# Kernel optimization log

Measured on AMD Instinct MI355X. Metric: run time of the kernel, lower is better.

The kernel has to match this reference:

```python
import jax, jax.numpy as jnp
import numpy as np

EPSILON = 1e-8
N, M, D = 8192, 8192, 128
NUM_LABELS = 10


def setup_inputs() -> dict:
    key = jax.random.key(0)
    k1, k2, k3 = jax.random.split(key, 3)
    a = jax.random.normal(k1, (N, D), dtype=jnp.float32)
    b = jax.random.normal(k2, (M, D), dtype=jnp.float32)
    labels_for_a = jax.random.randint(k3, (N,), 0, NUM_LABELS, dtype=jnp.int64)
    return {"a": a, "b": b, "labels_for_a": labels_for_a}


def reference(a, b, labels_for_a):
    d = a.shape[1]
    # p: [n, m] scaled similarity
    p = jnp.matmul(a, b.T) / jnp.sqrt(jnp.float32(d))
    ab = jax.nn.softmax(p, axis=1)        # [n, m] walk a->b
    ba = jax.nn.softmax(p.T, axis=1)      # [m, n] walk b->a
    aba = jnp.matmul(ab, ba)              # [n, n] round-trip probability
    # label-equality targets, normalized per row
    labels = labels_for_a[None, :]
    is_same_label = (labels == labels.T).astype(jnp.float32)  # [n, n]
    label_count = is_same_label.sum(axis=1, keepdims=True)
    targets = is_same_label / label_count
    walker_loss = -(targets * jnp.log(EPSILON + aba)).sum(axis=1).mean(axis=0)
    # visit loss: uniform target over b
    visit_probability = ab.mean(axis=0)   # [m]
    m = b.shape[0]
    uniform = jnp.float32(1.0 / m)
    visit_loss = -(uniform * jnp.log(EPSILON + visit_probability)).sum(axis=0)
    return (walker_loss, visit_loss)
```

## Files before the change

### kernel.cpp

```cpp
#include <hip/hip_runtime.h>


typedef __attribute__((ext_vector_type(8))) short bf16x8;
typedef __attribute__((ext_vector_type(4))) float f32x4;

#define NROW 8192
#define DIM 128
#define NLAB 10
#define EPSf 1e-8f
#define SF 0.35709582f
#define SPLIT 4
#define NPAIR 36
#define SPSTRIDE (360 * 16384)

#define O_WA 0
#define O_VA 8
#define O_CNT 64
#define O_OFF 128
#define O_SIDX 256
#define O_PS 33280
#define O_CS 557568
#define O_VK 590336
#define O_CV 623104
#define O_CKS 655872
#define O_ABF 688640
#define O_BBF 2785792
#define O_E 4882944
#define O_SP 139100672

__device__ __forceinline__ unsigned short f2bf(float f) {
  unsigned u = __builtin_bit_cast(unsigned, f);
  u += 0x7fffu + ((u >> 16) & 1u);
  return (unsigned short)(u >> 16);
}
__device__ __forceinline__ float bf2f(unsigned short s) {
  unsigned u = ((unsigned)s) << 16;
  return __builtin_bit_cast(float, u);
}

__global__ __launch_bounds__(256) void k_bucket(const int* __restrict__ lab,
                                                int* cnt, int* offs, int* sidx,
                                                double* wa, double* va,
                                                float* cs, float* vk) {
  __shared__ int lc[NLAB], lcur[NLAB];
  int tid = threadIdx.x;
  if (tid < NLAB) lc[tid] = 0;
  __syncthreads();
  for (int i = tid; i < NROW; i += 256) {
    int l = lab[i]; l = l < 0 ? 0 : (l > 9 ? 9 : l);
    atomicAdd(&lc[l], 1);
  }
  for (int i = tid; i < NROW; i += 256) { cs[i] = 0.f; vk[i] = 0.f; }
  __syncthreads();
  if (tid == 0) {
    int run = 0;
    for (int l = 0; l < NLAB; ++l) { cnt[l] = lc[l]; offs[l] = run; lcur[l] = run; run += lc[l]; }
    *wa = 0.0; *va = 0.0;
  }
  __syncthreads();
  for (int i = tid; i < NROW; i += 256) {
    int l = lab[i]; l = l < 0 ? 0 : (l > 9 ? 9 : l);
    int p = atomicAdd(&lcur[l], 1);
    sidx[p] = i;
  }
}

__global__ __launch_bounds__(256) void k_convert(const float* __restrict__ X,
                                                 unsigned short* __restrict__ Y) {
  int i = (blockIdx.x * 256 + threadIdx.x) * 8;
  f32x4 a = *(const f32x4*)(X + i);
  f32x4 b = *(const f32x4*)(X + i + 4);
  bf16x8 o;
  o[0] = (short)f2bf(a[0] * SF); o[1] = (short)f2bf(a[1] * SF);
  o[2] = (short)f2bf(a[2] * SF); o[3] = (short)f2bf(a[3] * SF);
  o[4] = (short)f2bf(b[0] * SF); o[5] = (short)f2bf(b[1] * SF);
  o[6] = (short)f2bf(b[2] * SF); o[7] = (short)f2bf(b[3] * SF);
  *(bf16x8*)(Y + i) = o;
}

__global__ __launch_bounds__(256, 2) void k_stats(const unsigned short* __restrict__ Abf,
                                                  const unsigned short* __restrict__ Bbf,
                                                  const int* __restrict__ sidx,
                                                  float* __restrict__ ps,
                                                  float* __restrict__ CS) {
  __shared__ int gidx[128];
  int tid = threadIdx.x;
  if (tid < 128) gidx[tid] = sidx[blockIdx.x * 128 + tid];
  __syncthreads();
  int wave = tid >> 6, lane = tid & 63;
  int wrow = wave >> 1, wcol = wave & 1;
  int m = lane & 15, quad = lane >> 4;
  bf16x8 af[4][4];
#pragma unroll
  for (int mi = 0; mi < 4; ++mi) {
    int gi = gidx[wrow * 64 + mi * 16 + m];
#pragma unroll
    for (int ks = 0; ks < 4; ++ks)
      af[mi][ks] = *(const bf16x8*)(Abf + gi * DIM + ks * 32 + quad * 8);
  }
  float tsum[4][4];
#pragma unroll
  for (int mi = 0; mi < 4; ++mi)
#pragma unroll
    for (int r = 0; r < 4; ++r) tsum[mi][r] = 0.f;
  int p0 = blockIdx.x * 128 + wrow * 64;
  for (int t = 0; t < 8; ++t) {
    int c0 = blockIdx.y * 1024 + t * 128 + wcol * 64;
    bf16x8 bfr[4][4];
#pragma unroll
    for (int ni = 0; ni < 4; ++ni)
#pragma unroll
      for (int ks = 0; ks < 4; ++ks)
        bfr[ni][ks] = *(const bf16x8*)(Bbf + (c0 + ni * 16 + m) * DIM + ks * 32 + quad * 8);
    f32x4 acc[4][4];
#pragma unroll
    for (int mi = 0; mi < 4; ++mi)
#pragma unroll
      for (int ni = 0; ni < 4; ++ni) acc[mi][ni] = (f32x4){0.f, 0.f, 0.f, 0.f};
#pragma unroll
    for (int ks = 0; ks < 4; ++ks)
#pragma unroll
      for (int mi = 0; mi < 4; ++mi)
#pragma unroll
        for (int ni = 0; ni < 4; ++ni)
          acc[mi][ni] = __builtin_amdgcn_mfma_f32_16x16x32_bf16(af[mi][ks], bfr[ni][ks], acc[mi][ni], 0, 0, 0);
    float csum[4] = {0.f, 0.f, 0.f, 0.f};
#pragma unroll
    for (int mi = 0; mi < 4; ++mi)
#pragma unroll
      for (int ni = 0; ni < 4; ++ni)
#pragma unroll
        for (int r = 0; r < 4; ++r) {
          float e = __builtin_amdgcn_exp2f(acc[mi][ni][r]);
          tsum[mi][r] += e;
          csum[ni] += e;
        }
#pragma unroll
    for (int ni = 0; ni < 4; ++ni) {
      csum[ni] += __shfl_xor(csum[ni], 16);
      csum[ni] += __shfl_xor(csum[ni], 32);
    }
    if (lane < 16) {
#pragma unroll
      for (int ni = 0; ni < 4; ++ni) atomicAdd(&CS[c0 + ni * 16 + lane], csum[ni]);
    }
  }
#pragma unroll
  for (int off = 1; off < 16; off <<= 1)
#pragma unroll
    for (int mi = 0; mi < 4; ++mi)
#pragma unroll
      for (int r = 0; r < 4; ++r) tsum[mi][r] += __shfl_xor(tsum[mi][r], off);
  if (m == 0) {
#pragma unroll
    for (int mi = 0; mi < 4; ++mi)
#pragma unroll
      for (int r = 0; r < 4; ++r)
        ps[(blockIdx.y * 2 + wcol) * NROW + p0 + mi * 16 + quad * 4 + r] = tsum[mi][r];
  }
}

__global__ __launch_bounds__(256) void k_mstats(const float* __restrict__ ps,
                                                const float* __restrict__ CS,
                                                float* __restrict__ CVs,
                                                float* __restrict__ CKS) {
  int i = blockIdx.x * 256 + threadIdx.x;
  float s = 0.f;
#pragma unroll
  for (int t = 0; t < 16; ++t) s += ps[t * NROW + i];
  CVs[i] = 1.f / s;
  CKS[i] = rsqrtf(CS[i]);
}

__global__ __launch_bounds__(256, 2) void k_fill(const unsigned short* __restrict__ Abf,
                                                 const unsigned short* __restrict__ Bbf,
                                                 const int* __restrict__ sidx,
                                                 const float* __restrict__ CVs,
                                                 const float* __restrict__ CKS,
                                                 unsigned short* __restrict__ E,
                                                 float* __restrict__ VK) {
  __shared__ int gidx[128];
  int tid = threadIdx.x;
  if (tid < 128) gidx[tid] = sidx[blockIdx.x * 128 + tid];
  __syncthreads();
  int wave = tid >> 6, lane = tid & 63;
  int wrow = wave >> 1, wcol = wave & 1;
  int m = lane & 15, quad = lane >> 4;
  int p0 = blockIdx.x * 128 + wrow * 64;
  bf16x8 af[4][4];
  float cv16[4][4];
#pragma unroll
  for (int mi = 0; mi < 4; ++mi) {
    int gi = gidx[wrow * 64 + mi * 16 + m];
#pragma unroll
    for (int ks = 0; ks < 4; ++ks)
      af[mi][ks] = *(const bf16x8*)(Abf + gi * DIM + ks * 32 + quad * 8);
#pragma unroll
    for (int r = 0; r < 4; ++r) cv16[mi][r] = CVs[p0 + mi * 16 + quad * 4 + r];
  }
  for (int t = 0; t < 8; ++t) {
    int c0 = blockIdx.y * 1024 + t * 128 + wcol * 64;
    bf16x8 bfr[4][4];
    float ck4[4];
#pragma unroll
    for (int ni = 0; ni < 4; ++ni) {
      ck4[ni] = CKS[c0 + ni * 16 + m];
#pragma unroll
      for (int ks = 0; ks < 4; ++ks)
        bfr[ni][ks] = *(const bf16x8*)(Bbf + (c0 + ni * 16 + m) * DIM + ks * 32 + quad * 8);
    }
    f32x4 acc[4][4];
#pragma unroll
    for (int mi = 0; mi < 4; ++mi)
#pragma unroll
      for (int ni = 0; ni < 4; ++ni) acc[mi][ni] = (f32x4){0.f, 0.f, 0.f, 0.f};
#pragma unroll
    for (int ks = 0; ks < 4; ++ks)
#pragma unroll
      for (int mi = 0; mi < 4; ++mi)
#pragma unroll
        for (int ni = 0; ni < 4; ++ni)
          acc[mi][ni] = __builtin_amdgcn_mfma_f32_16x16x32_bf16(af[mi][ks], bfr[ni][ks], acc[mi][ni], 0, 0, 0);
    float csum[4] = {0.f, 0.f, 0.f, 0.f};
#pragma unroll
    for (int mi = 0; mi < 4; ++mi)
#pragma unroll
      for (int ni = 0; ni < 4; ++ni)
#pragma unroll
        for (int r = 0; r < 4; ++r) {
          float e = __builtin_amdgcn_exp2f(acc[mi][ni][r]);
          int row = p0 + mi * 16 + quad * 4 + r;
          E[(size_t)row * NROW + c0 + ni * 16 + m] = f2bf(e * ck4[ni]);
          csum[ni] = fmaf(e, cv16[mi][r], csum[ni]);
        }
#pragma unroll
    for (int ni = 0; ni < 4; ++ni) {
      csum[ni] += __shfl_xor(csum[ni], 16);
      csum[ni] += __shfl_xor(csum[ni], 32);
    }
    if (lane < 16) {
#pragma unroll
      for (int ni = 0; ni < 4; ++ni) atomicAdd(&VK[c0 + ni * 16 + lane], csum[ni]);
    }
  }
}

__global__ __launch_bounds__(256) void k_vloss(const float* __restrict__ VK, double* va) {
  __shared__ float red[4];
  int tid = threadIdx.x;
  int i = blockIdx.x * 256 + tid;
  float l = __logf(EPSf + VK[i] * (1.f / 8192.f));
#pragma unroll
  for (int off = 32; off; off >>= 1) l += __shfl_down(l, off);
  if ((tid & 63) == 0) red[tid >> 6] = l;
  __syncthreads();
  if (tid == 0) {
    double tot = (double)red[0] + (double)red[1] + (double)red[2] + (double)red[3];
    atomicAdd(va, -tot / 8192.0);
  }
}

__global__ __launch_bounds__(256, 4) void k_gram(const unsigned short* __restrict__ Eh,
                                                 const int* __restrict__ cnt,
                                                 const int* __restrict__ offs,
                                                 unsigned short* __restrict__ Spart) {
  int gid = blockIdx.x;
  int xcd = gid & 7, slot = gid >> 3;
  int group = xcd * 5 + slot / NPAIR;
  int pidx = slot % NPAIR;
  int lab = group / SPLIT, split = group % SPLIT;
  int tj = 0;
  while ((tj + 1) * (tj + 2) / 2 <= pidx) ++tj;
  int ti = pidx - tj * (tj + 1) / 2;
  int c = cnt[lab], o = offs[lab];
  if (tj * 128 >= c) return;
  const bool diag = (ti == tj);
  __shared__ __align__(16) unsigned short Pt[128 * 64];
  __shared__ __align__(16) unsigned short Rt[128 * 64];
  int tid = threadIdx.x;
  int wave = tid >> 6, lane = tid & 63;
  int wrow = wave >> 1, wcol = wave & 1;
  int m = lane & 15, quad = lane >> 4;
  const unsigned short* pp[4];
  const unsigned short* pr[4];
  int lo[4];
#pragma unroll
  for (int v = 0; v < 4; ++v) {
    int slotv = v * 256 + tid, row = slotv >> 3, c8 = slotv & 7;
    int ri = o + ti * 128 + row; if (ri > NROW - 1) ri = NROW - 1;
    int rj = o + tj * 128 + row; if (rj > NROW - 1) rj = NROW - 1;
    pp[v] = Eh + (size_t)ri * NROW + split * 2048 + c8 * 8;
    pr[v] = Eh + (size_t)rj * NROW + split * 2048 + c8 * 8;
    lo[v] = row * 64 + ((c8 ^ (row & 7)) * 8);
  }
  f32x4 acc[4][4];
#pragma unroll
  for (int mi = 0; mi < 4; ++mi)
#pragma unroll
    for (int ni = 0; ni < 4; ++ni) acc[mi][ni] = (f32x4){0.f, 0.f, 0.f, 0.f};
  const unsigned short* Bt = diag ? Pt : Rt;
  for (int t = 0; t < 32; ++t) {
    __syncthreads();
    bf16x8 dp[4], dr[4];
#pragma unroll
    for (int v = 0; v < 4; ++v) {
      dp[v] = *(const bf16x8*)(pp[v]); pp[v] += 64;
      if (!diag) { dr[v] = *(const bf16x8*)(pr[v]); pr[v] += 64; }
    }
#pragma unroll
    for (int v = 0; v < 4; ++v) {
      *(bf16x8*)(Pt + lo[v]) = dp[v];
      if (!diag) *(bf16x8*)(Rt + lo[v]) = dr[v];
    }
    __syncthreads();
#pragma unroll
    for (int ks = 0; ks < 2; ++ks) {
      bf16x8 pa[4], rb[4];
#pragma unroll
      for (int mi = 0; mi < 4; ++mi) {
        int row = wrow * 64 + mi * 16 + m;
        pa[mi] = *(const bf16x8*)(Pt + row * 64 + (((ks * 4 + quad) ^ (row & 7)) * 8));
      }
#pragma unroll
      for (int ni = 0; ni < 4; ++ni) {
        int row = wcol * 64 + ni * 16 + m;
        rb[ni] = *(const bf16x8*)(Bt + row * 64 + (((ks * 4 + quad) ^ (row & 7)) * 8));
      }
#pragma unroll
      for (int mi = 0; mi < 4; ++mi)
#pragma unroll
        for (int ni = 0; ni < 4; ++ni)
          acc[mi][ni] = __builtin_amdgcn_mfma_f32_16x16x32_bf16(pa[mi], rb[ni], acc[mi][ni], 0, 0, 0);
    }
  }
  size_t base = (size_t)(split * SPSTRIDE) + (size_t)(lab * NPAIR + pidx) * 16384;
#pragma unroll
  for (int mi = 0; mi < 4; ++mi)
#pragma unroll
    for (int ni = 0; ni < 4; ++ni) {
      ushort4 w4;
      w4.x = f2bf(acc[mi][ni][0]);
      w4.y = f2bf(acc[mi][ni][1]);
      w4.z = f2bf(acc[mi][ni][2]);
      w4.w = f2bf(acc[mi][ni][3]);
      *(ushort4*)(Spart + base + (size_t)(mi * 4 + ni) * 1024 + tid * 4) = w4;
    }
}

__global__ __launch_bounds__(256) void k_reduce(const unsigned short* __restrict__ Spart,
                                                const int* __restrict__ cnt,
                                                const int* __restrict__ offs,
                                                const float* __restrict__ CVs,
                                                double* wa) {
  int lab = blockIdx.y, pidx = blockIdx.x;
  int tj = 0;
  while ((tj + 1) * (tj + 2) / 2 <= pidx) ++tj;
  int ti = pidx - tj * (tj + 1) / 2;
  int c = cnt[lab], o = offs[lab];
  if (tj * 128 >= c) return;
  __shared__ float isei[128], isej[128];
  __shared__ float red[4];
  int tid = threadIdx.x;
  if (tid < 128) {
    int ri = o + ti * 128 + tid; if (ri > NROW - 1) ri = NROW - 1;
    int rj = o + tj * 128 + tid; if (rj > NROW - 1) rj = NROW - 1;
    isei[tid] = CVs[ri];
    isej[tid] = CVs[rj];
  }
  __syncthreads();
  int wave = tid >> 6, lane = tid & 63;
  int wrow = wave >> 1, wcol = wave & 1;
  int m = lane & 15, quad = lane >> 4;
  size_t base = (size_t)(lab * NPAIR + pidx) * 16384;
  float lsum = 0.f;
#pragma unroll
  for (int mi = 0; mi < 4; ++mi)
#pragma unroll
    for (int ni = 0; ni < 4; ++ni) {
      size_t off = base + (size_t)(mi * 4 + ni) * 1024 + tid * 4;
      ushort4 s0 = *(const ushort4*)(Spart + off);
      ushort4 s1 = *(const ushort4*)(Spart + SPSTRIDE + off);
      ushort4 s2 = *(const ushort4*)(Spart + 2 * (size_t)SPSTRIDE + off);
      ushort4 s3 = *(const ushort4*)(Spart + 3 * (size_t)SPSTRIDE + off);
      float S[4];
      S[0] = bf2f(s0.x) + bf2f(s1.x) + bf2f(s2.x) + bf2f(s3.x);
      S[1] = bf2f(s0.y) + bf2f(s1.y) + bf2f(s2.y) + bf2f(s3.y);
      S[2] = bf2f(s0.z) + bf2f(s1.z) + bf2f(s2.z) + bf2f(s3.z);
      S[3] = bf2f(s0.w) + bf2f(s1.w) + bf2f(s2.w) + bf2f(s3.w);
      int jl = wcol * 64 + ni * 16 + m;
      int j = tj * 128 + jl;
#pragma unroll
      for (int r = 0; r < 4; ++r) {
        int il = wrow * 64 + mi * 16 + quad * 4 + r;
        int i = ti * 128 + il;
        if (i < c && j < c) {
          lsum += __logf(EPSf + S[r] * isei[il]);
          if (ti != tj) lsum += __logf(EPSf + S[r] * isej[jl]);
        }
      }
    }
#pragma unroll
  for (int off2 = 32; off2; off2 >>= 1) lsum += __shfl_down(lsum, off2);
  if (lane == 0) red[wave] = lsum;
  __syncthreads();
  if (tid == 0) {
    double tot = (double)red[0] + (double)red[1] + (double)red[2] + (double)red[3];
    atomicAdd(wa, -tot / (8192.0 * (double)c));
  }
}

__global__ void k_finish(const double* wa, const double* va, float* out) {
  out[0] = (float)(*wa);
  out[1] = (float)(*va);
}

extern "C" void kernel_launch(void* const* d_in, const int* in_sizes, int n_in,
                              void* d_out, int out_size, void* d_ws, size_t ws_size,
                              hipStream_t stream) {
  const float* A = (const float*)d_in[0];
  const float* B = (const float*)d_in[1];
  const int* LAB = (const int*)d_in[2];
  float* out = (float*)d_out;
  char* w = (char*)d_ws;
  double* WA = (double*)(w + O_WA);
  double* VA = (double*)(w + O_VA);
  int* CNT = (int*)(w + O_CNT);
  int* OFFS = (int*)(w + O_OFF);
  int* SIDX = (int*)(w + O_SIDX);
  float* PS = (float*)(w + O_PS);
  float* CS = (float*)(w + O_CS);
  float* VK = (float*)(w + O_VK);
  float* CVs = (float*)(w + O_CV);
  float* CKS = (float*)(w + O_CKS);
  unsigned short* ABF = (unsigned short*)(w + O_ABF);
  unsigned short* BBF = (unsigned short*)(w + O_BBF);
  unsigned short* E = (unsigned short*)(w + O_E);
  unsigned short* SP = (unsigned short*)(w + O_SP);

  k_bucket<<<1, 256, 0, stream>>>(LAB, CNT, OFFS, SIDX, WA, VA, CS, VK);
  k_convert<<<512, 256, 0, stream>>>(A, ABF);
  k_convert<<<512, 256, 0, stream>>>(B, BBF);
  k_stats<<<dim3(64, 8), 256, 0, stream>>>(ABF, BBF, SIDX, PS, CS);
  k_mstats<<<32, 256, 0, stream>>>(PS, CS, CVs, CKS);
  k_fill<<<dim3(64, 8), 256, 0, stream>>>(ABF, BBF, SIDX, CVs, CKS, E, VK);
  k_vloss<<<32, 256, 0, stream>>>(VK, VA);
  k_gram<<<NPAIR * SPLIT * NLAB, 256, 0, stream>>>(E, CNT, OFFS, SP);
  k_reduce<<<dim3(NPAIR, NLAB), 256, 0, stream>>>(SP, CNT, OFFS, CVs, WA);
  k_finish<<<1, 1, 0, stream>>>(WA, VA, out);
}
```

Baseline: 300.1 us.

## Prefetch next gram tile into registers and double stats/fill grid columns

The gram kernel now loads the next 64-column slice of E from global memory into registers while MFMAs run on the current shared-memory tile. This hides global load latency behind compute, at the cost of more registers, so occupancy drops from 4 to 3 blocks per SM. The stats and fill kernels split columns into 16 chunks of 512 instead of 8 of 1024, doubling the grid to improve occupancy. The partial-sum buffer and workspace offsets are enlarged to match.

```diff
diff --git a/kernel.cpp b/kernel.cpp
--- a/kernel.cpp
+++ b/kernel.cpp
@@ -19,14 +19,14 @@
 #define O_OFF 128
 #define O_SIDX 256
 #define O_PS 33280
-#define O_CS 557568
-#define O_VK 590336
-#define O_CV 623104
-#define O_CKS 655872
-#define O_ABF 688640
-#define O_BBF 2785792
-#define O_E 4882944
-#define O_SP 139100672
+#define O_CS 1081856
+#define O_VK 1114624
+#define O_CV 1147392
+#define O_CKS 1180160
+#define O_ABF 1212928
+#define O_BBF 3310080
+#define O_E 5407232
+#define O_SP 139624960
 
 __device__ __forceinline__ unsigned short f2bf(float f) {
   unsigned u = __builtin_bit_cast(unsigned, f);
@@ -104,8 +104,8 @@
 #pragma unroll
     for (int r = 0; r < 4; ++r) tsum[mi][r] = 0.f;
   int p0 = blockIdx.x * 128 + wrow * 64;
-  for (int t = 0; t < 8; ++t) {
-    int c0 = blockIdx.y * 1024 + t * 128 + wcol * 64;
+  for (int t = 0; t < 4; ++t) {
+    int c0 = blockIdx.y * 512 + t * 128 + wcol * 64;
     bf16x8 bfr[4][4];
 #pragma unroll
     for (int ni = 0; ni < 4; ++ni)
@@ -167,7 +167,7 @@
   int i = blockIdx.x * 256 + threadIdx.x;
   float s = 0.f;
 #pragma unroll
-  for (int t = 0; t < 16; ++t) s += ps[t * NROW + i];
+  for (int t = 0; t < 32; ++t) s += ps[t * NROW + i];
   CVs[i] = 1.f / s;
   CKS[i] = rsqrtf(CS[i]);
 }
@@ -198,8 +198,8 @@
 #pragma unroll
     for (int r = 0; r < 4; ++r) cv16[mi][r] = CVs[p0 + mi * 16 + quad * 4 + r];
   }
-  for (int t = 0; t < 8; ++t) {
-    int c0 = blockIdx.y * 1024 + t * 128 + wcol * 64;
+  for (int t = 0; t < 4; ++t) {
+    int c0 = blockIdx.y * 512 + t * 128 + wcol * 64;
     bf16x8 bfr[4][4];
     float ck4[4];
 #pragma unroll
@@ -260,7 +260,7 @@
   }
 }
 
-__global__ __launch_bounds__(256, 4) void k_gram(const unsigned short* __restrict__ Eh,
+__global__ __launch_bounds__(256, 3) void k_gram(const unsigned short* __restrict__ Eh,
                                                  const int* __restrict__ cnt,
                                                  const int* __restrict__ offs,
                                                  unsigned short* __restrict__ Spart) {
@@ -299,39 +299,61 @@
 #pragma unroll
     for (int ni = 0; ni < 4; ++ni) acc[mi][ni] = (f32x4){0.f, 0.f, 0.f, 0.f};
   const unsigned short* Bt = diag ? Pt : Rt;
-  for (int t = 0; t < 32; ++t) {
+  bf16x8 pA[4], rA[4], pB[4], rB[4];
+#pragma unroll
+  for (int v = 0; v < 4; ++v) {
+    pA[v] = *(const bf16x8*)(pp[v]); pp[v] += 64;
+    if (!diag) { rA[v] = *(const bf16x8*)(pr[v]); pr[v] += 64; }
+  }
+#define GRAM_MFMA_SECTION                                                     \
+  _Pragma("unroll")                                                           \
+  for (int ks = 0; ks < 2; ++ks) {                                            \
+    bf16x8 pa[4], rb[4];                                                      \
+    _Pragma("unroll")                                                         \
+    for (int mi = 0; mi < 4; ++mi) {                                          \
+      int row = wrow * 64 + mi * 16 + m;                                      \
+      pa[mi] = *(const bf16x8*)(Pt + row * 64 + (((ks * 4 + quad) ^ (row & 7)) * 8)); \
+    }                                                                         \
+    _Pragma("unroll")                                                         \
+    for (int ni = 0; ni < 4; ++ni) {                                          \
+      int row = wcol * 64 + ni * 16 + m;                                      \
+      rb[ni] = *(const bf16x8*)(Bt + row * 64 + (((ks * 4 + quad) ^ (row & 7)) * 8)); \
+    }                                                                         \
+    _Pragma("unroll")                                                         \
+    for (int mi = 0; mi < 4; ++mi)                                            \
+      _Pragma("unroll")                                                       \
+      for (int ni = 0; ni < 4; ++ni)                                          \
+        acc[mi][ni] = __builtin_amdgcn_mfma_f32_16x16x32_bf16(pa[mi], rb[ni], acc[mi][ni], 0, 0, 0); \
+  }
+  for (int t = 0; t < 32; t += 2) {
     __syncthreads();
-    bf16x8 dp[4], dr[4];
 #pragma unroll
     for (int v = 0; v < 4; ++v) {
-      dp[v] = *(const bf16x8*)(pp[v]); pp[v] += 64;
-      if (!diag) { dr[v] = *(const bf16x8*)(pr[v]); pr[v] += 64; }
-    }
+      *(bf16x8*)(Pt + lo[v]) = pA[v];
+      if (!diag) *(bf16x8*)(Rt + lo[v]) = rA[v];
+    }
+    __syncthreads();
 #pragma unroll
     for (int v = 0; v < 4; ++v) {
-      *(bf16x8*)(Pt + lo[v]) = dp[v];
-      if (!diag) *(bf16x8*)(Rt + lo[v]) = dr[v];
-    }
+      pB[v] = *(const bf16x8*)(pp[v]); pp[v] += 64;
+      if (!diag) { rB[v] = *(const bf16x8*)(pr[v]); pr[v] += 64; }
+    }
+    GRAM_MFMA_SECTION
     __syncthreads();
 #pragma unroll
-    for (int ks = 0; ks < 2; ++ks) {
-      bf16x8 pa[4], rb[4];
-#pragma unroll
-      for (int mi = 0; mi < 4; ++mi) {
-        int row = wrow * 64 + mi * 16 + m;
-        pa[mi] = *(const bf16x8*)(Pt + row * 64 + (((ks * 4 + quad) ^ (row & 7)) * 8));
+    for (int v = 0; v < 4; ++v) {
+      *(bf16x8*)(Pt + lo[v]) = pB[v];
+      if (!diag) *(bf16x8*)(Rt + lo[v]) = rB[v];
+    }
+    __syncthreads();
+    if (t + 2 < 32) {
+#pragma unroll
+      for (int v = 0; v < 4; ++v) {
+        pA[v] = *(const bf16x8*)(pp[v]); pp[v] += 64;
+        if (!diag) { rA[v] = *(const bf16x8*)(pr[v]); pr[v] += 64; }
       }
-#pragma unroll
-      for (int ni = 0; ni < 4; ++ni) {
-        int row = wcol * 64 + ni * 16 + m;
-        rb[ni] = *(const bf16x8*)(Bt + row * 64 + (((ks * 4 + quad) ^ (row & 7)) * 8));
-      }
-#pragma unroll
-      for (int mi = 0; mi < 4; ++mi)
-#pragma unroll
-        for (int ni = 0; ni < 4; ++ni)
-          acc[mi][ni] = __builtin_amdgcn_mfma_f32_16x16x32_bf16(pa[mi], rb[ni], acc[mi][ni], 0, 0, 0);
-    }
+    }
+    GRAM_MFMA_SECTION
   }
   size_t base = (size_t)(split * SPSTRIDE) + (size_t)(lab * NPAIR + pidx) * 16384;
 #pragma unroll
@@ -440,9 +462,9 @@
   k_bucket<<<1, 256, 0, stream>>>(LAB, CNT, OFFS, SIDX, WA, VA, CS, VK);
   k_convert<<<512, 256, 0, stream>>>(A, ABF);
   k_convert<<<512, 256, 0, stream>>>(B, BBF);
-  k_stats<<<dim3(64, 8), 256, 0, stream>>>(ABF, BBF, SIDX, PS, CS);
+  k_stats<<<dim3(64, 16), 256, 0, stream>>>(ABF, BBF, SIDX, PS, CS);
   k_mstats<<<32, 256, 0, stream>>>(PS, CS, CVs, CKS);
-  k_fill<<<dim3(64, 8), 256, 0, stream>>>(ABF, BBF, SIDX, CVs, CKS, E, VK);
+  k_fill<<<dim3(64, 16), 256, 0, stream>>>(ABF, BBF, SIDX, CVs, CKS, E, VK);
   k_vloss<<<32, 256, 0, stream>>>(VK, VA);
   k_gram<<<NPAIR * SPLIT * NLAB, 256, 0, stream>>>(E, CNT, OFFS, SP);
   k_reduce<<<dim3(NPAIR, NLAB), 256, 0, stream>>>(SP, CNT, OFFS, CVs, WA);
```

Result: slower. 450.0 us (+50.0%).
